# Performance work log

Measured on AMD Instinct MI355X. Metric: run time of the kernel, lower is better.

Reference implementation:

```python
import jax, jax.numpy as jnp
import numpy as np
import math

L, N, D = 1024, 64, 64
O = 1024

def setup_inputs() -> dict:
    key = jax.random.key(0)
    k1, k2 = jax.random.split(key)
    x = jax.random.normal(k1, (L, N, D), dtype=jnp.float32)
    upfold = jax.random.normal(k2, (O, N, D), dtype=jnp.float32)
    return {"x": x, "upfold": upfold}

def reference(x, upfold):
    # x: [L, N, D], upfold: [O, N, D]
    d = x.shape[-1]
    scale = 1.0 / math.sqrt(d)
    # affinities: [L, O, N]
    affinities = jnp.einsum('lnd,ond->lon', x, upfold) * scale
    # weighted sum with (sigmoid - 0.5) weights: [L, N, D]
    features = jnp.einsum('lon,ond->lnd', jax.nn.sigmoid(affinities) - 0.5, upfold)
    return features
```

## Files before the change

### kernel.cpp

```cpp
#include <hip/hip_runtime.h>
#include <stdint.h>

#define L_DIM 1024
#define N_DIM 64
#define D_DIM 64
#define O_DIM 1024
#define ND    4096
#define NT    8

typedef float    floatx16 __attribute__((ext_vector_type(16)));
typedef _Float16 half8    __attribute__((ext_vector_type(8)));
typedef _Float16 h2       __attribute__((ext_vector_type(2)));
typedef __fp16   fp16x2   __attribute__((ext_vector_type(2)));

#define UB_BYTES  9216
#define UTT_BYTES 9728
#define IMG_BYTES (UB_BYTES + UTT_BYTES)
#define WS_NEEDED ((size_t)N_DIM * 16 * IMG_BYTES)

#define BUF_STRIDE_FB 17920

__device__ __forceinline__ uint32_t pkh2(float a, float b) {
    fp16x2 p = __builtin_amdgcn_cvt_pkrtz(a, b);
    return __builtin_bit_cast(uint32_t, p);
}

__device__ __forceinline__ half8 mk_frag(uint32_t a, uint32_t b, uint32_t c, uint32_t d) {
    union { uint32_t u[4]; half8 v; } U;
    U.u[0] = a; U.u[1] = b; U.u[2] = c; U.u[3] = d;
    return U.v;
}

__device__ __forceinline__ uint32_t psig(float s0, float s1) {
    const h2 HI = {(_Float16)41.6f,        (_Float16)41.6f};
    const h2 LO = {(_Float16)-41.6f,       (_Float16)-41.6f};
    const h2 SC = {(_Float16)0.0625f,      (_Float16)0.0625f};
    const h2 C0 = {(_Float16)0.03099238f,  (_Float16)0.03099238f};
    const h2 C1 = {(_Float16)-0.00842090f, (_Float16)-0.00842090f};
    const h2 C2 = {(_Float16)0.00151845f,  (_Float16)0.00151845f};
    const h2 C3 = {(_Float16)-1.02197e-4f, (_Float16)-1.02197e-4f};
    h2 s = __builtin_bit_cast(h2, pkh2(s0, s1));
    s = __builtin_elementwise_min(s, HI);
    s = __builtin_elementwise_max(s, LO);
    h2 ha = s * SC;
    h2 v  = ha * ha;
    h2 w  = C2 + v * C3;
    w     = C1 + v * w;
    w     = C0 + v * w;
    h2 f  = s * w;
    return __builtin_bit_cast(uint32_t, f);
}

__device__ __forceinline__ void load_tile(const float* ubase, int ot,
                                          int r8, int c, float4* va, float4* vb) {
    const float* pr = ubase + (size_t)(ot * 64 + 2 * r8) * ND + 4 * c;
    #pragma unroll
    for (int j = 0; j < 2; ++j) {
        va[j] = *(const float4*)(pr + (size_t)(32 * j) * ND);
        vb[j] = *(const float4*)(pr + (size_t)(32 * j) * ND + ND);
    }
}

__global__ void __launch_bounds__(256)
conv_kernel(const float* __restrict__ up, unsigned char* __restrict__ img)
{
    const int tid = threadIdx.x;
    const int r8  = tid >> 4;
    const int c   = tid & 15;
    const int n   = blockIdx.x;
    const int ot  = blockIdx.y;

    const float* ubase = up + (size_t)n * D_DIM;
    float4 va[2], vb[2];
    load_tile(ubase, ot, r8, c, va, vb);

    unsigned char* tb = img + (size_t)(n * 16 + ot) * IMG_BYTES;
    uint16_t (*Ub)[72]  = (uint16_t (*)[72])tb;
    uint32_t (*UtT)[38] = (uint32_t (*)[38])(tb + UB_BYTES);

    #pragma unroll
    for (int j = 0; j < 2; ++j) {
        *(uint2*)&Ub[2*r8 + 32*j][4*c] =
            make_uint2(pkh2(va[j].x, va[j].y), pkh2(va[j].z, va[j].w));
        *(uint2*)&Ub[2*r8 + 32*j + 1][4*c] =
            make_uint2(pkh2(vb[j].x, vb[j].y), pkh2(vb[j].z, vb[j].w));
        const int op = r8 + 16*j;
        UtT[4*c + 0][op] = pkh2(va[j].x, vb[j].x);
        UtT[4*c + 1][op] = pkh2(va[j].y, vb[j].y);
        UtT[4*c + 2][op] = pkh2(va[j].z, vb[j].z);
        UtT[4*c + 3][op] = pkh2(va[j].w, vb[j].w);
    }
}

__global__ void __launch_bounds__(512, 4)
corr_kernel_r(const float* __restrict__ x, const unsigned char* __restrict__ img,
              float* __restrict__ out)
{
    __shared__ __align__(16) float Xs[128][68];

    const int tid  = threadIdx.x;
    const int lane = tid & 63;
    const int wid  = tid >> 6;
    const int team = wid >> 2;
    const int tw   = wid & 3;
    const int l31  = lane & 31;
    const int h    = lane >> 5;
    const int n    = blockIdx.x;
    const int lb   = blockIdx.y;
    const int lw   = lb * 128 + tw * 32 + l31;

    const unsigned char* gimg = img + (size_t)n * 16 * IMG_BYTES;

    half8 Xf[4];
    {
        const int xr = tid >> 2;
        const int xq = tid & 3;
        const float* xsrc = x + (size_t)(lb * 128 + xr) * ND + n * D_DIM;
        #pragma unroll
        for (int j = 0; j < 4; ++j) {
            const int f4i = xq * 4 + j;
            *(float4*)&Xs[xr][4 * f4i] = *(const float4*)(xsrc + 4 * f4i);
        }
        __syncthreads();
        const int rl = tw * 32 + l31;
        #pragma unroll
        for (int kk = 0; kk < 4; ++kk) {
            float4 f1 = *(const float4*)&Xs[rl][16 * kk + 8 * h];
            float4 f2 = *(const float4*)&Xs[rl][16 * kk + 8 * h + 4];
            Xf[kk] = mk_frag(pkh2(f1.x, f1.y), pkh2(f1.z, f1.w),
                             pkh2(f2.x, f2.y), pkh2(f2.z, f2.w));
        }
        __syncthreads();
    }

    floatx16 F0, F1;
    #pragma unroll
    for (int i = 0; i < 16; ++i) { F0[i] = 0.0f; F1[i] = 0.0f; }

    for (int ot = 0; ot < 16; ++ot) {
        const unsigned char* tb = gimg + (size_t)ot * IMG_BYTES;

        const unsigned char* ubp = tb + (size_t)(team * 32 + l31) * 144 + h * 16;
        half8 Ak[4];
        #pragma unroll
        for (int kk = 0; kk < 4; ++kk)
            Ak[kk] = *(const half8*)(ubp + kk * 32);

        floatx16 S;
        #pragma unroll
        for (int i2 = 0; i2 < 16; ++i2) S[i2] = 0.0f;
        #pragma unroll
        for (int kk = 0; kk < 4; ++kk)
            S = __builtin_amdgcn_mfma_f32_32x32x16_f16(Ak[kk], Xf[kk], S, 0, 0, 0);

        uint32_t P[8];
        #pragma unroll
        for (int m = 0; m < 8; ++m) P[m] = psig(S[2*m], S[2*m+1]);

        uint32_t R[4];
        #pragma unroll
        for (int c2 = 0; c2 < 2; ++c2) {
            const int t4 = c2 * 4;
            R[2*c2]   = __shfl_xor(h ? P[t4]     : P[t4 + 2], 32);
            R[2*c2+1] = __shfl_xor(h ? P[t4 + 1] : P[t4 + 3], 32);
        }
        const uint32_t* r0 = (const uint32_t*)(tb + UB_BYTES) + l31 * 38;
        const uint32_t* r1 = r0 + 32 * 38;
        #pragma unroll
        for (int c2 = 0; c2 < 2; ++c2) {
            const int t4 = c2 * 4;
            half8 B = h ? mk_frag(R[2*c2], R[2*c2+1], P[t4 + 2], P[t4 + 3])
                        : mk_frag(P[t4], P[t4 + 1], R[2*c2], R[2*c2+1]);
            const int opb = team * 16 + 8 * c2 + 4 * h;
            uint2 q0 = *(const uint2*)(r0 + opb);
            uint2 q1 = *(const uint2*)(r0 + opb + 2);
            uint2 q2 = *(const uint2*)(r1 + opb);
            uint2 q3 = *(const uint2*)(r1 + opb + 2);
            half8 A0 = mk_frag(q0.x, q0.y, q1.x, q1.y);
            half8 A1 = mk_frag(q2.x, q2.y, q3.x, q3.y);
            F0 = __builtin_amdgcn_mfma_f32_32x32x16_f16(A0, B, F0, 0, 0, 0);
            F1 = __builtin_amdgcn_mfma_f32_32x32x16_f16(A1, B, F1, 0, 0, 0);
        }
    }

    {
        const int row = tw * 32 + l31;
        if (team == 1) {
            #pragma unroll
            for (int q = 0; q < 4; ++q) {
                float4 a; a.x = F0[4*q]; a.y = F0[4*q+1]; a.z = F0[4*q+2]; a.w = F0[4*q+3];
                *(float4*)&Xs[row][8*q + 4*h] = a;
                float4 bq; bq.x = F1[4*q]; bq.y = F1[4*q+1]; bq.z = F1[4*q+2]; bq.w = F1[4*q+3];
                *(float4*)&Xs[row][32 + 8*q + 4*h] = bq;
            }
        }
        __syncthreads();
        if (team == 0) {
            float* op = out + (size_t)lw * ND + n * D_DIM;
            #pragma unroll
            for (int q = 0; q < 4; ++q) {
                float4 t0 = *(const float4*)&Xs[row][8*q + 4*h];
                float4 a; a.x = F0[4*q]   + t0.x; a.y = F0[4*q+1] + t0.y;
                          a.z = F0[4*q+2] + t0.z; a.w = F0[4*q+3] + t0.w;
                *(float4*)(op + 8*q + 4*h) = a;
                float4 t1 = *(const float4*)&Xs[row][32 + 8*q + 4*h];
                float4 bq; bq.x = F1[4*q]   + t1.x; bq.y = F1[4*q+1] + t1.y;
                           bq.z = F1[4*q+2] + t1.z; bq.w = F1[4*q+3] + t1.w;
                *(float4*)(op + 32 + 8*q + 4*h) = bq;
            }
        }
    }
}

__global__ void __launch_bounds__(512, 4)
corr_kernel_fb(const float* __restrict__ x, const float* __restrict__ up,
               float* __restrict__ out)
{
    __shared__ __align__(16) unsigned char smem[4 * BUF_STRIDE_FB];

    const int tid  = threadIdx.x;
    const int lane = tid & 63;
    const int wid  = tid >> 6;
    const int team = wid >> 2;
    const int tw   = wid & 3;
    const int l31  = lane & 31;
    const int h    = lane >> 5;
    const int ttid = tid & 255;
    const int r8   = ttid >> 4;
    const int c    = ttid & 15;
    const int n    = blockIdx.x;
    const int lb   = blockIdx.y;
    const int lw   = lb * 128 + tw * 32 + l31;

    const float* ubase = up + (size_t)n * D_DIM;
    const int ob = team * NT;
    unsigned char* tsmem = smem + team * 2 * BUF_STRIDE_FB;

    float4 va[2], vb[2];
    load_tile(ubase, ob + 0, r8, c, va, vb);

    half8 Xf[4];
    {
        float (*Xs)[68] = (float (*)[68])smem;
        const int xr = tid >> 2;
        const int xq = tid & 3;
        const float* xsrc = x + (size_t)(lb * 128 + xr) * ND + n * D_DIM;
        #pragma unroll
        for (int j = 0; j < 4; ++j) {
            const int f4i = xq * 4 + j;
            *(float4*)&Xs[xr][4 * f4i] = *(const float4*)(xsrc + 4 * f4i);
        }
        __syncthreads();
        const int rl = tw * 32 + l31;
        #pragma unroll
        for (int kk = 0; kk < 4; ++kk) {
            float4 f1 = *(const float4*)&Xs[rl][16 * kk + 8 * h];
            float4 f2 = *(const float4*)&Xs[rl][16 * kk + 8 * h + 4];
            Xf[kk] = mk_frag(pkh2(f1.x, f1.y), pkh2(f1.z, f1.w),
                             pkh2(f2.x, f2.y), pkh2(f2.z, f2.w));
        }
        __syncthreads();
    }

    #pragma unroll
    for (int j = 0; j < 2; ++j) {
        uint16_t (*Ub)[72]  = (uint16_t (*)[72])(tsmem);
        uint32_t (*Ut2)[68] = (uint32_t (*)[68])(tsmem + 9216);
        *(uint2*)&Ub[2*r8 + 32*j][4*c] =
            make_uint2(pkh2(va[j].x, va[j].y), pkh2(va[j].z, va[j].w));
        *(uint2*)&Ub[2*r8 + 32*j + 1][4*c] =
            make_uint2(pkh2(vb[j].x, vb[j].y), pkh2(vb[j].z, vb[j].w));
        *(uint4*)&Ut2[r8 + 16*j][4*c] =
            make_uint4(pkh2(va[j].x, vb[j].x), pkh2(va[j].y, vb[j].y),
                       pkh2(va[j].z, vb[j].z), pkh2(va[j].w, vb[j].w));
    }
    load_tile(ubase, ob + 1, r8, c, va, vb);
    __syncthreads();

    floatx16 F0, F1;
    #pragma unroll
    for (int i = 0; i < 16; ++i) { F0[i] = 0.0f; F1[i] = 0.0f; }

    for (int ot = 0; ot < NT; ++ot) {
        const int b = ot & 1;
        uint16_t (*Ub)[72]   = (uint16_t (*)[72])(tsmem + b * BUF_STRIDE_FB);
        const uint32_t* utp  = (const uint32_t*)(tsmem + b * BUF_STRIDE_FB + 9216);
        uint16_t (*Ubn)[72]  = (uint16_t (*)[72])(tsmem + (b ^ 1) * BUF_STRIDE_FB);
        uint32_t (*Ut2n)[68] = (uint32_t (*)[68])(tsmem + (b ^ 1) * BUF_STRIDE_FB + 9216);

        half8 A0k[4], A1k[4];
        #pragma unroll
        for (int kk = 0; kk < 4; ++kk) {
            A0k[kk] = *(const half8*)&Ub[l31][16 * kk + 8 * h];
            A1k[kk] = *(const half8*)&Ub[32 + l31][16 * kk + 8 * h];
        }

        if (ot + 1 < NT) {
            #pragma unroll
            for (int j = 0; j < 2; ++j) {
                *(uint2*)&Ubn[2*r8 + 32*j][4*c] =
                    make_uint2(pkh2(va[j].x, va[j].y), pkh2(va[j].z, va[j].w));
                *(uint2*)&Ubn[2*r8 + 32*j + 1][4*c] =
                    make_uint2(pkh2(vb[j].x, vb[j].y), pkh2(vb[j].z, vb[j].w));
                *(uint4*)&Ut2n[r8 + 16*j][4*c] =
                    make_uint4(pkh2(va[j].x, vb[j].x), pkh2(va[j].y, vb[j].y),
                               pkh2(va[j].z, vb[j].z), pkh2(va[j].w, vb[j].w));
            }
        }
        if (ot + 2 < NT)
            load_tile(ubase, ob + ot + 2, r8, c, va, vb);

        floatx16 S0, S1;
        #pragma unroll
        for (int i = 0; i < 16; ++i) { S0[i] = 0.0f; S1[i] = 0.0f; }
        #pragma unroll
        for (int kk = 0; kk < 4; ++kk) {
            S0 = __builtin_amdgcn_mfma_f32_32x32x16_f16(A0k[kk], Xf[kk], S0, 0, 0, 0);
            S1 = __builtin_amdgcn_mfma_f32_32x32x16_f16(A1k[kk], Xf[kk], S1, 0, 0, 0);
        }

        uint32_t P[16];
        #pragma unroll
        for (int m = 0; m < 8; ++m) P[m]     = psig(S0[2*m], S0[2*m+1]);
        #pragma unroll
        for (int m = 0; m < 8; ++m) P[8 + m] = psig(S1[2*m], S1[2*m+1]);

        uint32_t R[8];
        #pragma unroll
        for (int c2 = 0; c2 < 4; ++c2) {
            const uint32_t* Q = P + (c2 >> 1) * 8;
            const int t4 = (c2 & 1) * 4;
            R[2*c2]   = __shfl_xor(h ? Q[t4]     : Q[t4 + 2], 32);
            R[2*c2+1] = __shfl_xor(h ? Q[t4 + 1] : Q[t4 + 3], 32);
        }
        #pragma unroll
        for (int c2 = 0; c2 < 4; ++c2) {
            const uint32_t* Q = P + (c2 >> 1) * 8;
            const int t4 = (c2 & 1) * 4;
            half8 B = h ? mk_frag(R[2*c2], R[2*c2+1], Q[t4 + 2], Q[t4 + 3])
                        : mk_frag(Q[t4], Q[t4 + 1], R[2*c2], R[2*c2+1]);
            const int opb = 8 * c2 + 4 * h;
            uint32_t a0[4], a1[4];
            #pragma unroll
            for (int k = 0; k < 4; ++k) {
                a0[k] = utp[(opb + k) * 68 + l31];
                a1[k] = utp[(opb + k) * 68 + 32 + l31];
            }
            half8 A0 = mk_frag(a0[0], a0[1], a0[2], a0[3]);
            half8 A1 = mk_frag(a1[0], a1[1], a1[2], a1[3]);
            F0 = __builtin_amdgcn_mfma_f32_32x32x16_f16(A0, B, F0, 0, 0, 0);
            F1 = __builtin_amdgcn_mfma_f32_32x32x16_f16(A1, B, F1, 0, 0, 0);
        }
        __syncthreads();
    }

    {
        float (*Fs)[68] = (float (*)[68])smem;
        const int row = tw * 32 + l31;
        if (team == 1) {
            #pragma unroll
            for (int q = 0; q < 4; ++q) {
                float4 a; a.x = F0[4*q]; a.y = F0[4*q+1]; a.z = F0[4*q+2]; a.w = F0[4*q+3];
                *(float4*)&Fs[row][8*q + 4*h] = a;
                float4 bq; bq.x = F1[4*q]; bq.y = F1[4*q+1]; bq.z = F1[4*q+2]; bq.w = F1[4*q+3];
                *(float4*)&Fs[row][32 + 8*q + 4*h] = bq;
            }
        }
        __syncthreads();
        if (team == 0) {
            float* op = out + (size_t)lw * ND + n * D_DIM;
            #pragma unroll
            for (int q = 0; q < 4; ++q) {
                float4 t0 = *(const float4*)&Fs[row][8*q + 4*h];
                float4 a; a.x = F0[4*q]   + t0.x; a.y = F0[4*q+1] + t0.y;
                          a.z = F0[4*q+2] + t0.z; a.w = F0[4*q+3] + t0.w;
                *(float4*)(op + 8*q + 4*h) = a;
                float4 t1 = *(const float4*)&Fs[row][32 + 8*q + 4*h];
                float4 bq; bq.x = F1[4*q]   + t1.x; bq.y = F1[4*q+1] + t1.y;
                           bq.z = F1[4*q+2] + t1.z; bq.w = F1[4*q+3] + t1.w;
                *(float4*)(op + 32 + 8*q + 4*h) = bq;
            }
        }
    }
}

extern "C" void kernel_launch(void* const* d_in, const int* in_sizes, int n_in,
                              void* d_out, int out_size, void* d_ws, size_t ws_size,
                              hipStream_t stream)
{
    const float* x  = (const float*)d_in[0];
    const float* up = (const float*)d_in[1];
    float* out      = (float*)d_out;

    if (d_ws != nullptr && ws_size >= WS_NEEDED) {
        unsigned char* img = (unsigned char*)d_ws;
        conv_kernel<<<dim3(N_DIM, 16), dim3(256), 0, stream>>>(up, img);
        corr_kernel_r<<<dim3(N_DIM, L_DIM / 128), dim3(512), 0, stream>>>(x, img, out);
    } else {
        corr_kernel_fb<<<dim3(N_DIM, L_DIM / 128), dim3(512), 0, stream>>>(x, up, out);
    }
}
```

Measured before the change: 122.9 us.

## Pre-swizzle upfold image into MFMA fragment order for coalesced 16B loads

The preprocessing kernel now writes the fp16 upfold tiles in exactly the per-lane fragment order the MFMA instructions consume, so both operands load as contiguous 16-byte vectors per lane. It replaces the padded row-major and transposed layouts, which needed strided 8-byte loads and repacking. This should make the main kernel's global reads fully coalesced and cut load instruction count, but the conversion kernel now does scattered 4-byte writes to build the transposed image.

```diff
diff --git a/kernel.cpp b/kernel.cpp
--- a/kernel.cpp
+++ b/kernel.cpp
@@ -13,9 +13,7 @@
 typedef _Float16 h2       __attribute__((ext_vector_type(2)));
 typedef __fp16   fp16x2   __attribute__((ext_vector_type(2)));
 
-#define UB_BYTES  9216
-#define UTT_BYTES 9728
-#define IMG_BYTES (UB_BYTES + UTT_BYTES)
+#define IMG_BYTES 16384
 #define WS_NEEDED ((size_t)N_DIM * 16 * IMG_BYTES)
 
 #define BUF_STRIDE_FB 17920
@@ -75,25 +73,43 @@
     load_tile(ubase, ot, r8, c, va, vb);
 
     unsigned char* tb = img + (size_t)(n * 16 + ot) * IMG_BYTES;
-    uint16_t (*Ub)[72]  = (uint16_t (*)[72])tb;
-    uint32_t (*UtT)[38] = (uint32_t (*)[38])(tb + UB_BYTES);
-
+
+    const int kk = c >> 2;
+    const int hh = (c >> 1) & 1;
+    const int co = (c & 1) * 8;
     #pragma unroll
     for (int j = 0; j < 2; ++j) {
-        *(uint2*)&Ub[2*r8 + 32*j][4*c] =
+        const int o0 = 2 * r8 + 32 * j;
+        unsigned char* g1 = tb + j * 4096 + kk * 1024 + co;
+        *(uint2*)(g1 + ((o0 & 31) + 32 * hh) * 16) =
             make_uint2(pkh2(va[j].x, va[j].y), pkh2(va[j].z, va[j].w));
-        *(uint2*)&Ub[2*r8 + 32*j + 1][4*c] =
+        *(uint2*)(g1 + (((o0 + 1) & 31) + 32 * hh) * 16) =
             make_uint2(pkh2(vb[j].x, vb[j].y), pkh2(vb[j].z, vb[j].w));
-        const int op = r8 + 16*j;
-        UtT[4*c + 0][op] = pkh2(va[j].x, vb[j].x);
-        UtT[4*c + 1][op] = pkh2(va[j].y, vb[j].y);
-        UtT[4*c + 2][op] = pkh2(va[j].z, vb[j].z);
-        UtT[4*c + 3][op] = pkh2(va[j].w, vb[j].w);
+    }
+
+    #pragma unroll
+    for (int j = 0; j < 2; ++j) {
+        const int op   = r8 + 16 * j;
+        const int g    = op >> 2;
+        const int slot = op & 3;
+        const int t2   = g >> 2;
+        const int c22  = (g >> 1) & 1;
+        const int h2i  = g & 1;
+        const float* pa = (const float*)&va[j];
+        const float* pb = (const float*)&vb[j];
+        #pragma unroll
+        for (int col = 0; col < 4; ++col) {
+            const int d   = 4 * c + col;
+            const int r   = d >> 5;
+            const int lane = (d & 31) + 32 * h2i;
+            *(uint32_t*)(tb + 8192 + t2 * 4096 + c22 * 2048 + r * 1024
+                         + lane * 16 + slot * 4) = pkh2(pa[col], pb[col]);
+        }
     }
 }
 
 __global__ void __launch_bounds__(512, 4)
-corr_kernel_r(const float* __restrict__ x, const unsigned char* __restrict__ img,
+corr_kernel_c(const float* __restrict__ x, const unsigned char* __restrict__ img,
               float* __restrict__ out)
 {
     __shared__ __align__(16) float Xs[128][68];
@@ -140,11 +156,11 @@
     for (int ot = 0; ot < 16; ++ot) {
         const unsigned char* tb = gimg + (size_t)ot * IMG_BYTES;
 
-        const unsigned char* ubp = tb + (size_t)(team * 32 + l31) * 144 + h * 16;
+        const unsigned char* g1 = tb + team * 4096 + lane * 16;
         half8 Ak[4];
         #pragma unroll
         for (int kk = 0; kk < 4; ++kk)
-            Ak[kk] = *(const half8*)(ubp + kk * 32);
+            Ak[kk] = *(const half8*)(g1 + kk * 1024);
 
         floatx16 S;
         #pragma unroll
@@ -164,20 +180,14 @@
             R[2*c2]   = __shfl_xor(h ? P[t4]     : P[t4 + 2], 32);
             R[2*c2+1] = __shfl_xor(h ? P[t4 + 1] : P[t4 + 3], 32);
         }
-        const uint32_t* r0 = (const uint32_t*)(tb + UB_BYTES) + l31 * 38;
-        const uint32_t* r1 = r0 + 32 * 38;
+        const unsigned char* g2 = tb + 8192 + team * 4096 + lane * 16;
         #pragma unroll
         for (int c2 = 0; c2 < 2; ++c2) {
             const int t4 = c2 * 4;
             half8 B = h ? mk_frag(R[2*c2], R[2*c2+1], P[t4 + 2], P[t4 + 3])
                         : mk_frag(P[t4], P[t4 + 1], R[2*c2], R[2*c2+1]);
-            const int opb = team * 16 + 8 * c2 + 4 * h;
-            uint2 q0 = *(const uint2*)(r0 + opb);
-            uint2 q1 = *(const uint2*)(r0 + opb + 2);
-            uint2 q2 = *(const uint2*)(r1 + opb);
-            uint2 q3 = *(const uint2*)(r1 + opb + 2);
-            half8 A0 = mk_frag(q0.x, q0.y, q1.x, q1.y);
-            half8 A1 = mk_frag(q2.x, q2.y, q3.x, q3.y);
+            half8 A0 = *(const half8*)(g2 + c2 * 2048);
+            half8 A1 = *(const half8*)(g2 + c2 * 2048 + 1024);
             F0 = __builtin_amdgcn_mfma_f32_32x32x16_f16(A0, B, F0, 0, 0, 0);
             F1 = __builtin_amdgcn_mfma_f32_32x32x16_f16(A1, B, F1, 0, 0, 0);
         }
@@ -395,7 +405,7 @@
     if (d_ws != nullptr && ws_size >= WS_NEEDED) {
         unsigned char* img = (unsigned char*)d_ws;
         conv_kernel<<<dim3(N_DIM, 16), dim3(256), 0, stream>>>(up, img);
-        corr_kernel_r<<<dim3(N_DIM, L_DIM / 128), dim3(512), 0, stream>>>(x, img, out);
+        corr_kernel_c<<<dim3(N_DIM, L_DIM / 128), dim3(512), 0, stream>>>(x, img, out);
     } else {
         corr_kernel_fb<<<dim3(N_DIM, L_DIM / 128), dim3(512), 0, stream>>>(x, up, out);
     }
```

Result: faster. 111.6 us (-9.2%).
